# Performance work log

Measured on AMD Instinct MI355X. Metric: run time of the kernel, lower is better.

Reference implementation:

```python
import jax, jax.numpy as jnp
import numpy as np

HIDDEN = 32


def setup_inputs() -> dict:
    key = jax.random.key(0)
    ks = jax.random.split(key, 8)
    B, T, I = 1024, 512, 64
    s_ih = 1.0 / np.sqrt(HIDDEN)
    return {
        "x": jax.random.normal(ks[0], (B, T, I), dtype=jnp.float32),
        "h0": jnp.zeros((1, B, HIDDEN), dtype=jnp.float32),
        "W_ih": jax.random.uniform(ks[1], (HIDDEN, I), jnp.float32, -s_ih, s_ih),
        "b_ih": jax.random.uniform(ks[2], (HIDDEN,), jnp.float32, -s_ih, s_ih),
        "W_hh": jax.random.uniform(ks[3], (HIDDEN, HIDDEN), jnp.float32, -s_ih, s_ih),
        "b_hh": jax.random.uniform(ks[4], (HIDDEN,), jnp.float32, -s_ih, s_ih),
        "W_out": jax.random.uniform(ks[5], (1, HIDDEN), jnp.float32, -s_ih, s_ih),
        "b_out": jax.random.uniform(ks[6], (1,), jnp.float32, -s_ih, s_ih),
    }


def reference(x, h0, W_ih, b_ih, W_hh, b_hh, W_out, b_out):
    # x: [B, T, I]; h0: [1, B, H] (num_layers=1)
    # Precompute input contribution for all timesteps in one GEMM: [B, T, H]
    x_proj = jnp.einsum("bti,hi->bth", x, W_ih) + b_ih

    def step(h, xt):  # h: [B, H], xt: [B, H]
        h_new = jnp.tanh(xt + h @ W_hh.T + b_hh)
        return h_new, h_new

    h_last, r_out_t = jax.lax.scan(step, h0[0], jnp.swapaxes(x_proj, 0, 1))
    r_out = jnp.swapaxes(r_out_t, 0, 1)  # [B, T, H]
    # Per-timestep Linear(32 -> 1), batched as one GEMM: [B, T, 1]
    outs = r_out @ W_out.T + b_out
    return outs, h_last[None]
```

## Files before the change

### kernel.cpp

```cpp
#include <hip/hip_runtime.h>

#define Bc 1024
#define Tc 512
#define Ic 64
#define Hc 32
#define L2E2 2.8853900817779268f

#define XT_ROW 24
#define XT_BUF (Hc * XT_ROW)

typedef __bf16 bf16x8 __attribute__((ext_vector_type(8)));
typedef __bf16 bf16x4 __attribute__((ext_vector_type(4)));
typedef float  f32x4  __attribute__((ext_vector_type(4)));
typedef _Float16 half2v __attribute__((ext_vector_type(2)));
typedef unsigned uint2v __attribute__((ext_vector_type(2)));

__device__ inline bf16x8 to_bf16x8(float4 u0, float4 u1) {
    bf16x8 t;
    t[0] = (__bf16)u0.x; t[1] = (__bf16)u0.y; t[2] = (__bf16)u0.z; t[3] = (__bf16)u0.w;
    t[4] = (__bf16)u1.x; t[5] = (__bf16)u1.y; t[6] = (__bf16)u1.z; t[7] = (__bf16)u1.w;
    return t;
}
__device__ inline bf16x8 to_bf16x8s(float4 u0, float4 u1, float s) {
    bf16x8 t;
    t[0] = (__bf16)(u0.x*s); t[1] = (__bf16)(u0.y*s); t[2] = (__bf16)(u0.z*s); t[3] = (__bf16)(u0.w*s);
    t[4] = (__bf16)(u1.x*s); t[5] = (__bf16)(u1.y*s); t[6] = (__bf16)(u1.z*s); t[7] = (__bf16)(u1.w*s);
    return t;
}


#define RORD(dst, src, N)                                                     \
    dst = (unsigned)__builtin_amdgcn_mov_dpp((int)(src), 0x120 + (N), 0xF, 0xF, false);

#if __has_builtin(__builtin_amdgcn_permlane16_swap)
#define PLSWAP(A, B)                                                          \
    { uint2v _t = __builtin_amdgcn_permlane16_swap((A), (B), false, false);   \
      (A) = _t[0]; (B) = _t[1]; }
#else
#define PLSWAP(A, B)                                                          \
    asm("s_nop 1\n\tv_permlane16_swap_b32 %0, %1" : "+v"(A), "+v"(B));
#endif

#if __has_builtin(__builtin_amdgcn_permlane32_swap)
#define P32SWAP(A, B)                                                         \
    { uint2v _t = __builtin_amdgcn_permlane32_swap((A), (B), false, false);   \
      (A) = _t[0]; (B) = _t[1]; }
#else
#define P32SWAP(A, B)                                                         \
    asm("s_nop 1\n\tv_permlane32_swap_b32 %0, %1" : "+v"(A), "+v"(B));
#endif

#if __has_builtin(__builtin_amdgcn_fdot2)
#define FDOT(g, W, a)                                                         \
    __builtin_amdgcn_fdot2(__builtin_bit_cast(half2v, (unsigned)(g)), (W), (a), false)
#else
__device__ inline float fdot2_emul(unsigned g, half2v w, float a) {
    half2v v = __builtin_bit_cast(half2v, g);
    a = fmaf((float)v[0], (float)w[0], a);
    return fmaf((float)v[1], (float)w[1], a);
}
#define FDOT(g, W, a) fdot2_emul((g), (W), (a))
#endif

#define STEP(xv, uu)                                                          \
    {                                                                         \
        unsigned c8;                                                          \
        RORD(c8, c, 8)                                                        \
        const unsigned bse = rlo ? c : c8;                                    \
        unsigned g1, g2, g3, g4, g5, g6, g7;                                  \
        RORD(g1, bse, 1) RORD(g2, bse, 2) RORD(g3, bse, 3) RORD(g4, bse, 4)   \
        RORD(g5, bse, 5) RORD(g6, bse, 6) RORD(g7, bse, 7)                    \
        float a0 = FDOT(bse, W0, (xv));                                       \
        float a1 = FDOT(g1,  W1, bch);                                        \
        a0 = FDOT(g2, W2, a0);  a1 = FDOT(g3, W3, a1);                        \
        a0 = FDOT(g4, W4, a0);  a1 = FDOT(g5, W5, a1);                        \
        a0 = FDOT(g6, W6, a0);  a1 = FDOT(g7, W7, a1);                        \
        const float Ah = a0 + a1;                                             \
        unsigned sa = __builtin_bit_cast(unsigned, Ah), sb2 = sa;             \
        P32SWAP(sa, sb2)                                                      \
        const float A = __builtin_bit_cast(float, sa) +                       \
                        __builtin_bit_cast(float, sb2);                       \
        const float p_ = __builtin_amdgcn_exp2f(A);                           \
        rr = __builtin_amdgcn_rcpf(p_ + 1.0f);                                \
        pbuf[uu][hh] = fmaf(rr, w2o, wo);                                     \
        unsigned P0 = __builtin_bit_cast(unsigned, rr), P1 = P0;              \
        PLSWAP(P0, P1)                                                        \
        const float rrp = __builtin_bit_cast(float, psel ? P0 : P1);          \
        const float ev = rodd ? rrp : rr;                                     \
        const float od = rodd ? rr : rrp;                                     \
        c = __builtin_bit_cast(unsigned, __builtin_amdgcn_cvt_pkrtz(ev, od)); \
    }

#define CVT8(dlo, dhi, src)                                                   \
    dlo.x = (float)(src)[0]; dlo.y = (float)(src)[1];                         \
    dlo.z = (float)(src)[2]; dlo.w = (float)(src)[3];                         \
    dhi.x = (float)(src)[4]; dhi.y = (float)(src)[5];                         \
    dhi.z = (float)(src)[6]; dhi.w = (float)(src)[7];

#define TILE_LOAD(lt)                                                         \
    do {                                                                      \
        const float* xp_ = x + ((size_t)b * Tc + (lt) * 16 + m2) * Ic + r * 8;\
        Xa0 = ((const float4*)xp_)[0];                                        \
        Xa1 = ((const float4*)xp_)[1];                                        \
        Xa2 = ((const float4*)(xp_ + 32))[0];                                 \
        Xa3 = ((const float4*)(xp_ + 32))[1];                                 \
    } while (0)

#define TILE_MFMA(tp)                                                         \
    do {                                                                      \
        const bf16x8 A0_ = to_bf16x8(Xa0, Xa1);                               \
        const bf16x8 A1_ = to_bf16x8(Xa2, Xa3);                               \
        f32x4 ac0 = {0.f, 0.f, 0.f, 0.f};                                     \
        f32x4 ac1 = {0.f, 0.f, 0.f, 0.f};                                     \
        ac0 = __builtin_amdgcn_mfma_f32_16x16x32_bf16(A0_, Bf[0][0], ac0, 0, 0, 0); \
        ac0 = __builtin_amdgcn_mfma_f32_16x16x32_bf16(A1_, Bf[0][1], ac0, 0, 0, 0); \
        ac1 = __builtin_amdgcn_mfma_f32_16x16x32_bf16(A0_, Bf[1][0], ac1, 0, 0, 0); \
        ac1 = __builtin_amdgcn_mfma_f32_16x16x32_bf16(A1_, Bf[1][1], ac1, 0, 0, 0); \
        bf16x4 p0_, p1_;                                                      \
        p0_[0] = (__bf16)(ac0[0] + bias0); p0_[1] = (__bf16)(ac0[1] + bias0); \
        p0_[2] = (__bf16)(ac0[2] + bias0); p0_[3] = (__bf16)(ac0[3] + bias0); \
        p1_[0] = (__bf16)(ac1[0] + bias1); p1_[1] = (__bf16)(ac1[1] + bias1); \
        p1_[2] = (__bf16)(ac1[2] + bias1); p1_[3] = (__bf16)(ac1[3] + bias1); \
        *(bf16x4*)&(tp)[m2 * XT_ROW + r * 4]        = p0_;                    \
        *(bf16x4*)&(tp)[(m2 + 16) * XT_ROW + r * 4] = p1_;                    \
    } while (0)

__global__ __launch_bounds__(64, 1) void fused_rnn_kernel(
    const float* __restrict__ x, const float* __restrict__ Wih,
    const float* __restrict__ bih, const float* __restrict__ h0,
    const float* __restrict__ Whh, const float* __restrict__ bhh,
    const float* __restrict__ Wout, const float* __restrict__ bout,
    float* __restrict__ out)
{
    __shared__ __bf16 xt[2 * XT_BUF];
    __shared__ float  pbuf[16][36];

    const int lane = threadIdx.x;
    const int m2   = lane & 15;
    const int r    = lane >> 4;
    const bool rlo  = (lane < 32);
    const bool rodd = (r & 1);
    const int  hh   = 2 * m2 + (r & 1);
    const int  b    = blockIdx.x;

    const float shalf = 0.5f * L2E2;
    bf16x8 Bf[2][2];
#pragma unroll
    for (int nh = 0; nh < 2; ++nh)
#pragma unroll
        for (int kh = 0; kh < 2; ++kh) {
            const float* wp = Wih + (m2 + 16 * nh) * Ic + r * 8 + kh * 32;
            Bf[nh][kh] = to_bf16x8s(((const float4*)wp)[0],
                                    ((const float4*)wp)[1], shalf);
        }
    const float bias0 = bih[m2] * shalf;
    const float bias1 = bih[m2 + 16] * shalf;

    bool psel;
    {
        unsigned d0 = (unsigned)lane, d1 = (unsigned)lane;
        PLSWAP(d0, d1)
        psel = (d0 == (unsigned)(lane ^ 16));
    }

    unsigned s0p = (unsigned)(2 * m2) | ((unsigned)(2 * m2 + 1) << 16);
    unsigned s8p;
    RORD(s8p, s0p, 8)
    const unsigned sbp = rlo ? s0p : s8p;
    unsigned sk1, sk2, sk3, sk4, sk5, sk6, sk7;
    RORD(sk1, sbp, 1) RORD(sk2, sbp, 2) RORD(sk3, sbp, 3) RORD(sk4, sbp, 4)
    RORD(sk5, sbp, 5) RORD(sk6, sbp, 6) RORD(sk7, sbp, 7)

    const float cw = -2.0f * L2E2;
    const float* wrh = Whh + hh * Hc;
#define MKW(Wk, sk)                                                           \
    half2v Wk;                                                                \
    {                                                                         \
        const unsigned jl_ = (sk) & 0xFFFFu, jh_ = (sk) >> 16;                \
        Wk[0] = (_Float16)(wrh[jl_] * cw);                                    \
        Wk[1] = (_Float16)(wrh[jh_] * cw);                                    \
    }
    MKW(W0, sbp) MKW(W1, sk1) MKW(W2, sk2) MKW(W3, sk3)
    MKW(W4, sk4) MKW(W5, sk5) MKW(W6, sk6) MKW(W7, sk7)
#undef MKW

    float rs = 0.f;
#pragma unroll
    for (int j = 0; j < Hc; ++j) rs += wrh[j];
    const float bch = (bhh[hh] + rs) * shalf;
    const float wo  = Wout[hh];
    const float w2o = -2.0f * wo;
    const float bo  = bout[0];

    const float h0e = h0[(size_t)b * Hc + 2 * m2];
    const float h0o = h0[(size_t)b * Hc + 2 * m2 + 1];
    const float re0 = fmaf(-0.5f, h0e, 0.5f);
    const float ro0 = fmaf(-0.5f, h0o, 0.5f);
    unsigned c = __builtin_bit_cast(unsigned, __builtin_amdgcn_cvt_pkrtz(re0, ro0));
    float rr = rodd ? ro0 : re0;
    float* orow = out + (size_t)b * Tc;

    float4 Xa0, Xa1, Xa2, Xa3;
    TILE_LOAD(0);
    TILE_MFMA(xt);
    TILE_LOAD(1);
    TILE_MFMA(xt + XT_BUF);
    TILE_LOAD(2);
    __syncthreads();

    const __bf16* xrbase = xt + hh * XT_ROW;

    bf16x8 na0 = *(const bf16x8*)(xrbase), na1 = *(const bf16x8*)(xrbase + 8);
    float4 qa0, qa1, qa2, qa3;
    CVT8(qa0, qa1, na0) CVT8(qa2, qa3, na1)

#pragma unroll 1
    for (int tb = 0; tb < Tc / 16; ++tb) {
        const int tbn = (tb + 1 < Tc / 16) ? tb + 1 : tb;
        const __bf16* xr = xrbase + (tbn & 1) * XT_BUF;
        na0 = *(const bf16x8*)(xr); na1 = *(const bf16x8*)(xr + 8);

        if (tb + 2 < Tc / 16) { TILE_MFMA(xt + (tb & 1) * XT_BUF); }
        if (tb + 3 < Tc / 16) { TILE_LOAD(tb + 3); }

        STEP(qa0.x, 0)  STEP(qa0.y, 1)  STEP(qa0.z, 2)  STEP(qa0.w, 3)
        STEP(qa1.x, 4)  STEP(qa1.y, 5)  STEP(qa1.z, 6)  STEP(qa1.w, 7)
        STEP(qa2.x, 8)  STEP(qa2.y, 9)  STEP(qa2.z, 10) STEP(qa2.w, 11)
        STEP(qa3.x, 12) STEP(qa3.y, 13) STEP(qa3.z, 14) STEP(qa3.w, 15)

        __builtin_amdgcn_wave_barrier();

        if (lane < 16) {
            const float4* pr = (const float4*)&pbuf[lane][0];
            const float4 s0_ = pr[0], s1_ = pr[1], s2_ = pr[2], s3_ = pr[3];
            const float4 s4_ = pr[4], s5_ = pr[5], s6_ = pr[6], s7_ = pr[7];
            const float s =
                ((((s0_.x + s0_.y) + (s0_.z + s0_.w)) +
                  ((s1_.x + s1_.y) + (s1_.z + s1_.w))) +
                 (((s2_.x + s2_.y) + (s2_.z + s2_.w)) +
                  ((s3_.x + s3_.y) + (s3_.z + s3_.w)))) +
                ((((s4_.x + s4_.y) + (s4_.z + s4_.w)) +
                  ((s5_.x + s5_.y) + (s5_.z + s5_.w))) +
                 (((s6_.x + s6_.y) + (s6_.z + s6_.w)) +
                  ((s7_.x + s7_.y) + (s7_.z + s7_.w))));
            orow[tb * 16 + lane] = s + bo;
        }
        __builtin_amdgcn_wave_barrier();

        CVT8(qa0, qa1, na0) CVT8(qa2, qa3, na1)
    }

    out[(size_t)Bc * Tc + (size_t)b * Hc + hh] = fmaf(-2.0f, rr, 1.0f);
}

extern "C" void kernel_launch(void* const* d_in, const int* in_sizes, int n_in,
                              void* d_out, int out_size, void* d_ws, size_t ws_size,
                              hipStream_t stream) {
    const float* x    = (const float*)d_in[0];
    const float* h0   = (const float*)d_in[1];
    const float* Wih  = (const float*)d_in[2];
    const float* bih  = (const float*)d_in[3];
    const float* Whh  = (const float*)d_in[4];
    const float* bhh  = (const float*)d_in[5];
    const float* Wout = (const float*)d_in[6];
    const float* bout = (const float*)d_in[7];
    float* out = (float*)d_out;

    fused_rnn_kernel<<<Bc, 64, 0, stream>>>(x, Wih, bih, h0, Whh, bhh,
                                            Wout, bout, out);
}
```

Measured before the change: 225.2 us.

## Split recurrence and projection into producer/consumer waves with fp32 DPP dot

Launches two waves per block. Wave 1 produces the bf16 MFMA input projection and reduces the output linear for the previous tile, while wave 0 runs only the serial recurrence. The recurrence now uses full-fp32 FMAs on 32 lanes with DPP rotations and a permlane16 swap, in place of packed fp16 dot products followed by a cross-half permlane32 reduction. This takes the projection and output work off the serial critical path and removes the half-precision packing. In exchange it adds a block-wide __syncthreads every 16 timesteps and more DPP moves per step.

```diff
diff --git a/kernel.cpp b/kernel.cpp
--- a/kernel.cpp
+++ b/kernel.cpp
@@ -12,7 +12,6 @@
 typedef __bf16 bf16x8 __attribute__((ext_vector_type(8)));
 typedef __bf16 bf16x4 __attribute__((ext_vector_type(4)));
 typedef float  f32x4  __attribute__((ext_vector_type(4)));
-typedef _Float16 half2v __attribute__((ext_vector_type(2)));
 typedef unsigned uint2v __attribute__((ext_vector_type(2)));
 
 __device__ inline bf16x8 to_bf16x8(float4 u0, float4 u1) {
@@ -41,54 +40,60 @@
     asm("s_nop 1\n\tv_permlane16_swap_b32 %0, %1" : "+v"(A), "+v"(B));
 #endif
 
-#if __has_builtin(__builtin_amdgcn_permlane32_swap)
-#define P32SWAP(A, B)                                                         \
-    { uint2v _t = __builtin_amdgcn_permlane32_swap((A), (B), false, false);   \
-      (A) = _t[0]; (B) = _t[1]; }
-#else
-#define P32SWAP(A, B)                                                         \
-    asm("s_nop 1\n\tv_permlane32_swap_b32 %0, %1" : "+v"(A), "+v"(B));
-#endif
-
-#if __has_builtin(__builtin_amdgcn_fdot2)
-#define FDOT(g, W, a)                                                         \
-    __builtin_amdgcn_fdot2(__builtin_bit_cast(half2v, (unsigned)(g)), (W), (a), false)
-#else
-__device__ inline float fdot2_emul(unsigned g, half2v w, float a) {
-    half2v v = __builtin_bit_cast(half2v, g);
-    a = fmaf((float)v[0], (float)w[0], a);
-    return fmaf((float)v[1], (float)w[1], a);
-}
-#define FDOT(g, W, a) fdot2_emul((g), (W), (a))
-#endif
+#define F32(u) __builtin_bit_cast(float, (u))
 
 #define STEP(xv, uu)                                                          \
     {                                                                         \
-        unsigned c8;                                                          \
-        RORD(c8, c, 8)                                                        \
-        const unsigned bse = rlo ? c : c8;                                    \
-        unsigned g1, g2, g3, g4, g5, g6, g7;                                  \
-        RORD(g1, bse, 1) RORD(g2, bse, 2) RORD(g3, bse, 3) RORD(g4, bse, 4)   \
-        RORD(g5, bse, 5) RORD(g6, bse, 6) RORD(g7, bse, 7)                    \
-        float a0 = FDOT(bse, W0, (xv));                                       \
-        float a1 = FDOT(g1,  W1, bch);                                        \
-        a0 = FDOT(g2, W2, a0);  a1 = FDOT(g3, W3, a1);                        \
-        a0 = FDOT(g4, W4, a0);  a1 = FDOT(g5, W5, a1);                        \
-        a0 = FDOT(g6, W6, a0);  a1 = FDOT(g7, W7, a1);                        \
-        const float Ah = a0 + a1;                                             \
-        unsigned sa = __builtin_bit_cast(unsigned, Ah), sb2 = sa;             \
-        P32SWAP(sa, sb2)                                                      \
-        const float A = __builtin_bit_cast(float, sa) +                       \
-                        __builtin_bit_cast(float, sb2);                       \
-        const float p_ = __builtin_amdgcn_exp2f(A);                           \
-        rr = __builtin_amdgcn_rcpf(p_ + 1.0f);                                \
-        pbuf[uu][hh] = fmaf(rr, w2o, wo);                                     \
-        unsigned P0 = __builtin_bit_cast(unsigned, rr), P1 = P0;              \
-        PLSWAP(P0, P1)                                                        \
-        const float rrp = __builtin_bit_cast(float, psel ? P0 : P1);          \
-        const float ev = rodd ? rrp : rr;                                     \
-        const float od = rodd ? rr : rrp;                                     \
-        c = __builtin_bit_cast(unsigned, __builtin_amdgcn_cvt_pkrtz(ev, od)); \
+        unsigned P0_ = c, P1_ = c;                                            \
+        PLSWAP(P0_, P1_)                                                      \
+        const unsigned cp = psel ? P0_ : P1_;                                 \
+        unsigned o1,o2,o3,o4,o5,o6,o7,o8,o9,o10,o11,o12,o13,o14,o15;          \
+        unsigned p1,p2,p3,p4,p5,p6,p7,p8,p9,p10,p11,p12,p13,p14,p15;          \
+        RORD(o1,c,1)  RORD(o2,c,2)   RORD(o3,c,3)   RORD(o4,c,4)              \
+        RORD(o5,c,5)  RORD(o6,c,6)   RORD(o7,c,7)   RORD(o8,c,8)              \
+        RORD(o9,c,9)  RORD(o10,c,10) RORD(o11,c,11) RORD(o12,c,12)            \
+        RORD(o13,c,13) RORD(o14,c,14) RORD(o15,c,15)                          \
+        RORD(p1,cp,1)  RORD(p2,cp,2)   RORD(p3,cp,3)   RORD(p4,cp,4)          \
+        RORD(p5,cp,5)  RORD(p6,cp,6)   RORD(p7,cp,7)   RORD(p8,cp,8)          \
+        RORD(p9,cp,9)  RORD(p10,cp,10) RORD(p11,cp,11) RORD(p12,cp,12)        \
+        RORD(p13,cp,13) RORD(p14,cp,14) RORD(p15,cp,15)                       \
+        float a0 = fmaf(F32(c), Wo0, (xv));                                   \
+        a0 = fmaf(F32(o1), Wo1, a0);                                          \
+        a0 = fmaf(F32(o2), Wo2, a0);                                          \
+        a0 = fmaf(F32(o3), Wo3, a0);                                          \
+        float a1 = F32(o4) * Wo4;                                             \
+        a1 = fmaf(F32(o5), Wo5, a1);                                          \
+        a1 = fmaf(F32(o6), Wo6, a1);                                          \
+        a1 = fmaf(F32(o7), Wo7, a1);                                          \
+        float a2 = F32(o8) * Wo8;                                             \
+        a2 = fmaf(F32(o9),  Wo9,  a2);                                        \
+        a2 = fmaf(F32(o10), Wo10, a2);                                        \
+        a2 = fmaf(F32(o11), Wo11, a2);                                        \
+        float a3 = F32(o12) * Wo12;                                           \
+        a3 = fmaf(F32(o13), Wo13, a3);                                        \
+        a3 = fmaf(F32(o14), Wo14, a3);                                        \
+        a3 = fmaf(F32(o15), Wo15, a3);                                        \
+        float a4 = fmaf(F32(cp), Wp0, bch);                                   \
+        a4 = fmaf(F32(p1), Wp1, a4);                                          \
+        a4 = fmaf(F32(p2), Wp2, a4);                                          \
+        a4 = fmaf(F32(p3), Wp3, a4);                                          \
+        float a5 = F32(p4) * Wp4;                                             \
+        a5 = fmaf(F32(p5), Wp5, a5);                                          \
+        a5 = fmaf(F32(p6), Wp6, a5);                                          \
+        a5 = fmaf(F32(p7), Wp7, a5);                                          \
+        float a6 = F32(p8) * Wp8;                                             \
+        a6 = fmaf(F32(p9),  Wp9,  a6);                                        \
+        a6 = fmaf(F32(p10), Wp10, a6);                                        \
+        a6 = fmaf(F32(p11), Wp11, a6);                                        \
+        float a7 = F32(p12) * Wp12;                                           \
+        a7 = fmaf(F32(p13), Wp13, a7);                                        \
+        a7 = fmaf(F32(p14), Wp14, a7);                                        \
+        a7 = fmaf(F32(p15), Wp15, a7);                                        \
+        const float A_ = ((a0 + a1) + (a2 + a3)) + ((a4 + a5) + (a6 + a7));   \
+        const float e_ = __builtin_amdgcn_exp2f(A_);                          \
+        rr = __builtin_amdgcn_rcpf(e_ + 1.0f);                                \
+        pb[(uu) * 36] = fmaf(rr, w2o, wo);                                    \
+        c = __builtin_bit_cast(unsigned, rr);                                 \
     }
 
 #define CVT8(dlo, dhi, src)                                                   \
@@ -125,7 +130,7 @@
         *(bf16x4*)&(tp)[(m2 + 16) * XT_ROW + r * 4] = p1_;                    \
     } while (0)
 
-__global__ __launch_bounds__(64, 1) void fused_rnn_kernel(
+__global__ __launch_bounds__(128, 1) void fused_rnn_kernel(
     const float* __restrict__ x, const float* __restrict__ Wih,
     const float* __restrict__ bih, const float* __restrict__ h0,
     const float* __restrict__ Whh, const float* __restrict__ bhh,
@@ -133,124 +138,158 @@
     float* __restrict__ out)
 {
     __shared__ __bf16 xt[2 * XT_BUF];
-    __shared__ float  pbuf[16][36];
-
-    const int lane = threadIdx.x;
+    __shared__ float  pbuf[2][16][36];
+
+    const int tid  = threadIdx.x;
+    const int wid  = tid >> 6;
+    const int lane = tid & 63;
     const int m2   = lane & 15;
     const int r    = lane >> 4;
-    const bool rlo  = (lane < 32);
-    const bool rodd = (r & 1);
-    const int  hh   = 2 * m2 + (r & 1);
-    const int  b    = blockIdx.x;
-
-    const float shalf = 0.5f * L2E2;
+    const int h31  = lane & 31;
+    const int b    = blockIdx.x;
+
     bf16x8 Bf[2][2];
+    float  bias0 = 0.f, bias1 = 0.f;
+    float4 Xa0, Xa1, Xa2, Xa3;
+    bool  psel = false;
+    float Wo0=0,Wo1=0,Wo2=0,Wo3=0,Wo4=0,Wo5=0,Wo6=0,Wo7=0,
+          Wo8=0,Wo9=0,Wo10=0,Wo11=0,Wo12=0,Wo13=0,Wo14=0,Wo15=0,
+          Wp0=0,Wp1=0,Wp2=0,Wp3=0,Wp4=0,Wp5=0,Wp6=0,Wp7=0,
+          Wp8=0,Wp9=0,Wp10=0,Wp11=0,Wp12=0,Wp13=0,Wp14=0,Wp15=0;
+    float bch = 0.f, wo = 0.f, w2o = 0.f, rr = 0.f;
+    unsigned c = 0;
+    bf16x8 na0, na1;
+    float4 qa0, qa1, qa2, qa3;
+    const float bo = bout[0];
+    float* orow = out + (size_t)b * Tc;
+    const __bf16* xrbase = xt + h31 * XT_ROW;
+
+    if (wid == 1) {
 #pragma unroll
-    for (int nh = 0; nh < 2; ++nh)
+        for (int nh = 0; nh < 2; ++nh)
 #pragma unroll
-        for (int kh = 0; kh < 2; ++kh) {
-            const float* wp = Wih + (m2 + 16 * nh) * Ic + r * 8 + kh * 32;
-            Bf[nh][kh] = to_bf16x8s(((const float4*)wp)[0],
-                                    ((const float4*)wp)[1], shalf);
+            for (int kh = 0; kh < 2; ++kh) {
+                const float* wp = Wih + (m2 + 16 * nh) * Ic + r * 8 + kh * 32;
+                Bf[nh][kh] = to_bf16x8s(((const float4*)wp)[0],
+                                        ((const float4*)wp)[1], L2E2);
+            }
+        bias0 = bih[m2] * L2E2;
+        bias1 = bih[m2 + 16] * L2E2;
+        TILE_LOAD(0); TILE_MFMA(xt);
+        TILE_LOAD(1); TILE_MFMA(xt + XT_BUF);
+        TILE_LOAD(2);
+    } else {
+        {
+            unsigned d0 = (unsigned)lane, d1 = (unsigned)lane;
+            PLSWAP(d0, d1)
+            psel = (d0 == (unsigned)(lane ^ 16));
         }
-    const float bias0 = bih[m2] * shalf;
-    const float bias1 = bih[m2 + 16] * shalf;
-
-    bool psel;
-    {
-        unsigned d0 = (unsigned)lane, d1 = (unsigned)lane;
-        PLSWAP(d0, d1)
-        psel = (d0 == (unsigned)(lane ^ 16));
-    }
-
-    unsigned s0p = (unsigned)(2 * m2) | ((unsigned)(2 * m2 + 1) << 16);
-    unsigned s8p;
-    RORD(s8p, s0p, 8)
-    const unsigned sbp = rlo ? s0p : s8p;
-    unsigned sk1, sk2, sk3, sk4, sk5, sk6, sk7;
-    RORD(sk1, sbp, 1) RORD(sk2, sbp, 2) RORD(sk3, sbp, 3) RORD(sk4, sbp, 4)
-    RORD(sk5, sbp, 5) RORD(sk6, sbp, 6) RORD(sk7, sbp, 7)
-
-    const float cw = -2.0f * L2E2;
-    const float* wrh = Whh + hh * Hc;
-#define MKW(Wk, sk)                                                           \
-    half2v Wk;                                                                \
-    {                                                                         \
-        const unsigned jl_ = (sk) & 0xFFFFu, jh_ = (sk) >> 16;                \
-        Wk[0] = (_Float16)(wrh[jl_] * cw);                                    \
-        Wk[1] = (_Float16)(wrh[jh_] * cw);                                    \
-    }
-    MKW(W0, sbp) MKW(W1, sk1) MKW(W2, sk2) MKW(W3, sk3)
-    MKW(W4, sk4) MKW(W5, sk5) MKW(W6, sk6) MKW(W7, sk7)
-#undef MKW
-
-    float rs = 0.f;
+        const unsigned u = (unsigned)h31;
+        unsigned up;
+        { unsigned U0 = u, U1 = u; PLSWAP(U0, U1) up = psel ? U0 : U1; }
+        unsigned so1,so2,so3,so4,so5,so6,so7,so8,so9,so10,so11,so12,so13,so14,so15;
+        unsigned sp1,sp2,sp3,sp4,sp5,sp6,sp7,sp8,sp9,sp10,sp11,sp12,sp13,sp14,sp15;
+        RORD(so1,u,1)  RORD(so2,u,2)   RORD(so3,u,3)   RORD(so4,u,4)
+        RORD(so5,u,5)  RORD(so6,u,6)   RORD(so7,u,7)   RORD(so8,u,8)
+        RORD(so9,u,9)  RORD(so10,u,10) RORD(so11,u,11) RORD(so12,u,12)
+        RORD(so13,u,13) RORD(so14,u,14) RORD(so15,u,15)
+        RORD(sp1,up,1)  RORD(sp2,up,2)   RORD(sp3,up,3)   RORD(sp4,up,4)
+        RORD(sp5,up,5)  RORD(sp6,up,6)   RORD(sp7,up,7)   RORD(sp8,up,8)
+        RORD(sp9,up,9)  RORD(sp10,up,10) RORD(sp11,up,11) RORD(sp12,up,12)
+        RORD(sp13,up,13) RORD(sp14,up,14) RORD(sp15,up,15)
+        const float cw = -2.0f * L2E2;
+        const float* wrh = Whh + h31 * Hc;
+        Wo0  = wrh[u]    * cw;
+        Wo1  = wrh[so1]  * cw;  Wo2  = wrh[so2]  * cw;
+        Wo3  = wrh[so3]  * cw;  Wo4  = wrh[so4]  * cw;
+        Wo5  = wrh[so5]  * cw;  Wo6  = wrh[so6]  * cw;
+        Wo7  = wrh[so7]  * cw;  Wo8  = wrh[so8]  * cw;
+        Wo9  = wrh[so9]  * cw;  Wo10 = wrh[so10] * cw;
+        Wo11 = wrh[so11] * cw;  Wo12 = wrh[so12] * cw;
+        Wo13 = wrh[so13] * cw;  Wo14 = wrh[so14] * cw;
+        Wo15 = wrh[so15] * cw;
+        Wp0  = wrh[up]   * cw;
+        Wp1  = wrh[sp1]  * cw;  Wp2  = wrh[sp2]  * cw;
+        Wp3  = wrh[sp3]  * cw;  Wp4  = wrh[sp4]  * cw;
+        Wp5  = wrh[sp5]  * cw;  Wp6  = wrh[sp6]  * cw;
+        Wp7  = wrh[sp7]  * cw;  Wp8  = wrh[sp8]  * cw;
+        Wp9  = wrh[sp9]  * cw;  Wp10 = wrh[sp10] * cw;
+        Wp11 = wrh[sp11] * cw;  Wp12 = wrh[sp12] * cw;
+        Wp13 = wrh[sp13] * cw;  Wp14 = wrh[sp14] * cw;
+        Wp15 = wrh[sp15] * cw;
+        float rs = 0.f;
 #pragma unroll
-    for (int j = 0; j < Hc; ++j) rs += wrh[j];
-    const float bch = (bhh[hh] + rs) * shalf;
-    const float wo  = Wout[hh];
-    const float w2o = -2.0f * wo;
-    const float bo  = bout[0];
-
-    const float h0e = h0[(size_t)b * Hc + 2 * m2];
-    const float h0o = h0[(size_t)b * Hc + 2 * m2 + 1];
-    const float re0 = fmaf(-0.5f, h0e, 0.5f);
-    const float ro0 = fmaf(-0.5f, h0o, 0.5f);
-    unsigned c = __builtin_bit_cast(unsigned, __builtin_amdgcn_cvt_pkrtz(re0, ro0));
-    float rr = rodd ? ro0 : re0;
-    float* orow = out + (size_t)b * Tc;
-
-    float4 Xa0, Xa1, Xa2, Xa3;
-    TILE_LOAD(0);
-    TILE_MFMA(xt);
-    TILE_LOAD(1);
-    TILE_MFMA(xt + XT_BUF);
-    TILE_LOAD(2);
+        for (int j = 0; j < Hc; ++j) rs += wrh[j];
+        bch = (bhh[h31] + rs) * L2E2;
+        wo  = Wout[h31];
+        w2o = -2.0f * wo;
+        rr = fmaf(-0.5f, h0[(size_t)b * Hc + h31], 0.5f);
+        c  = __builtin_bit_cast(unsigned, rr);
+    }
     __syncthreads();
 
-    const __bf16* xrbase = xt + hh * XT_ROW;
-
-    bf16x8 na0 = *(const bf16x8*)(xrbase), na1 = *(const bf16x8*)(xrbase + 8);
-    float4 qa0, qa1, qa2, qa3;
-    CVT8(qa0, qa1, na0) CVT8(qa2, qa3, na1)
+    if (wid == 0) {
+        na0 = *(const bf16x8*)(xrbase);
+        na1 = *(const bf16x8*)(xrbase + 8);
+        CVT8(qa0, qa1, na0) CVT8(qa2, qa3, na1)
+    }
+    __syncthreads();
 
 #pragma unroll 1
     for (int tb = 0; tb < Tc / 16; ++tb) {
-        const int tbn = (tb + 1 < Tc / 16) ? tb + 1 : tb;
-        const __bf16* xr = xrbase + (tbn & 1) * XT_BUF;
-        na0 = *(const bf16x8*)(xr); na1 = *(const bf16x8*)(xr + 8);
-
-        if (tb + 2 < Tc / 16) { TILE_MFMA(xt + (tb & 1) * XT_BUF); }
-        if (tb + 3 < Tc / 16) { TILE_LOAD(tb + 3); }
-
-        STEP(qa0.x, 0)  STEP(qa0.y, 1)  STEP(qa0.z, 2)  STEP(qa0.w, 3)
-        STEP(qa1.x, 4)  STEP(qa1.y, 5)  STEP(qa1.z, 6)  STEP(qa1.w, 7)
-        STEP(qa2.x, 8)  STEP(qa2.y, 9)  STEP(qa2.z, 10) STEP(qa2.w, 11)
-        STEP(qa3.x, 12) STEP(qa3.y, 13) STEP(qa3.z, 14) STEP(qa3.w, 15)
-
-        __builtin_amdgcn_wave_barrier();
-
-        if (lane < 16) {
-            const float4* pr = (const float4*)&pbuf[lane][0];
-            const float4 s0_ = pr[0], s1_ = pr[1], s2_ = pr[2], s3_ = pr[3];
-            const float4 s4_ = pr[4], s5_ = pr[5], s6_ = pr[6], s7_ = pr[7];
-            const float s =
-                ((((s0_.x + s0_.y) + (s0_.z + s0_.w)) +
-                  ((s1_.x + s1_.y) + (s1_.z + s1_.w))) +
-                 (((s2_.x + s2_.y) + (s2_.z + s2_.w)) +
-                  ((s3_.x + s3_.y) + (s3_.z + s3_.w)))) +
-                ((((s4_.x + s4_.y) + (s4_.z + s4_.w)) +
-                  ((s5_.x + s5_.y) + (s5_.z + s5_.w))) +
-                 (((s6_.x + s6_.y) + (s6_.z + s6_.w)) +
-                  ((s7_.x + s7_.y) + (s7_.z + s7_.w))));
-            orow[tb * 16 + lane] = s + bo;
+        if (wid == 0) {
+            const int tbn = (tb + 1 < Tc / 16) ? tb + 1 : tb;
+            const __bf16* xr = xrbase + (tbn & 1) * XT_BUF;
+            na0 = *(const bf16x8*)(xr);
+            na1 = *(const bf16x8*)(xr + 8);
+
+            float* pb = &pbuf[tb & 1][0][h31];
+            STEP(qa0.x, 0)  STEP(qa0.y, 1)  STEP(qa0.z, 2)  STEP(qa0.w, 3)
+            STEP(qa1.x, 4)  STEP(qa1.y, 5)  STEP(qa1.z, 6)  STEP(qa1.w, 7)
+            STEP(qa2.x, 8)  STEP(qa2.y, 9)  STEP(qa2.z, 10) STEP(qa2.w, 11)
+            STEP(qa3.x, 12) STEP(qa3.y, 13) STEP(qa3.z, 14) STEP(qa3.w, 15)
+
+            CVT8(qa0, qa1, na0) CVT8(qa2, qa3, na1)
+        } else {
+            if (tb + 2 < Tc / 16) { TILE_MFMA(xt + (tb & 1) * XT_BUF); }
+            if (tb + 3 < Tc / 16) { TILE_LOAD(tb + 3); }
+            if (tb >= 1 && lane < 16) {
+                const float4* pr = (const float4*)&pbuf[(tb - 1) & 1][lane][0];
+                const float4 s0_ = pr[0], s1_ = pr[1], s2_ = pr[2], s3_ = pr[3];
+                const float4 s4_ = pr[4], s5_ = pr[5], s6_ = pr[6], s7_ = pr[7];
+                const float s =
+                    ((((s0_.x + s0_.y) + (s0_.z + s0_.w)) +
+                      ((s1_.x + s1_.y) + (s1_.z + s1_.w))) +
+                     (((s2_.x + s2_.y) + (s2_.z + s2_.w)) +
+                      ((s3_.x + s3_.y) + (s3_.z + s3_.w)))) +
+                    ((((s4_.x + s4_.y) + (s4_.z + s4_.w)) +
+                      ((s5_.x + s5_.y) + (s5_.z + s5_.w))) +
+                     (((s6_.x + s6_.y) + (s6_.z + s6_.w)) +
+                      ((s7_.x + s7_.y) + (s7_.z + s7_.w))));
+                orow[(tb - 1) * 16 + lane] = s + bo;
+            }
         }
-        __builtin_amdgcn_wave_barrier();
-
-        CVT8(qa0, qa1, na0) CVT8(qa2, qa3, na1)
-    }
-
-    out[(size_t)Bc * Tc + (size_t)b * Hc + hh] = fmaf(-2.0f, rr, 1.0f);
+        __syncthreads();
+    }
+
+    if (wid == 1 && lane < 16) {
+        const float4* pr = (const float4*)&pbuf[(Tc / 16 - 1) & 1][lane][0];
+        const float4 s0_ = pr[0], s1_ = pr[1], s2_ = pr[2], s3_ = pr[3];
+        const float4 s4_ = pr[4], s5_ = pr[5], s6_ = pr[6], s7_ = pr[7];
+        const float s =
+            ((((s0_.x + s0_.y) + (s0_.z + s0_.w)) +
+              ((s1_.x + s1_.y) + (s1_.z + s1_.w))) +
+             (((s2_.x + s2_.y) + (s2_.z + s2_.w)) +
+              ((s3_.x + s3_.y) + (s3_.z + s3_.w)))) +
+            ((((s4_.x + s4_.y) + (s4_.z + s4_.w)) +
+              ((s5_.x + s5_.y) + (s5_.z + s5_.w))) +
+             (((s6_.x + s6_.y) + (s6_.z + s6_.w)) +
+              ((s7_.x + s7_.y) + (s7_.z + s7_.w))));
+        orow[(Tc / 16 - 1) * 16 + lane] = s + bo;
+    }
+    if (wid == 0 && lane < 32) {
+        out[(size_t)Bc * Tc + (size_t)b * Hc + lane] = fmaf(-2.0f, rr, 1.0f);
+    }
 }
 
 extern "C" void kernel_launch(void* const* d_in, const int* in_sizes, int n_in,
@@ -266,6 +305,6 @@
     const float* bout = (const float*)d_in[7];
     float* out = (float*)d_out;
 
-    fused_rnn_kernel<<<Bc, 64, 0, stream>>>(x, Wih, bih, h0, Whh, bhh,
-                                            Wout, bout, out);
+    fused_rnn_kernel<<<Bc, 128, 0, stream>>>(x, Wih, bih, h0, Whh, bhh,
+                                             Wout, bout, out);
 }
```

Result: slower. 236.0 us (+4.8%).

## Compute full recurrent dot per lane with 16 DPP rotations, drop cross-half swap

Applied to the files above, without the earlier changes.

Each lane now computes the whole 32-element recurrent dot product itself, using 15 row-rotate DPP moves and 16 fdot2 ops across four accumulator chains. Previously the two wave halves each computed half the sum and combined them with a permlane32 swap. This removes the cross-half exchange and add from the serial per-timestep critical path, and the 0.5 scale factors are folded into L2E2. The cost is more DPP and fdot2 work per step, plus redundant computation across the two halves, so only lanes below 32 write the final hidden state.

```diff
diff --git a/kernel.cpp b/kernel.cpp
--- a/kernel.cpp
+++ b/kernel.cpp
@@ -41,15 +41,6 @@
     asm("s_nop 1\n\tv_permlane16_swap_b32 %0, %1" : "+v"(A), "+v"(B));
 #endif
 
-#if __has_builtin(__builtin_amdgcn_permlane32_swap)
-#define P32SWAP(A, B)                                                         \
-    { uint2v _t = __builtin_amdgcn_permlane32_swap((A), (B), false, false);   \
-      (A) = _t[0]; (B) = _t[1]; }
-#else
-#define P32SWAP(A, B)                                                         \
-    asm("s_nop 1\n\tv_permlane32_swap_b32 %0, %1" : "+v"(A), "+v"(B));
-#endif
-
 #if __has_builtin(__builtin_amdgcn_fdot2)
 #define FDOT(g, W, a)                                                         \
     __builtin_amdgcn_fdot2(__builtin_bit_cast(half2v, (unsigned)(g)), (W), (a), false)
@@ -64,23 +55,23 @@
 
 #define STEP(xv, uu)                                                          \
     {                                                                         \
-        unsigned c8;                                                          \
-        RORD(c8, c, 8)                                                        \
-        const unsigned bse = rlo ? c : c8;                                    \
-        unsigned g1, g2, g3, g4, g5, g6, g7;                                  \
-        RORD(g1, bse, 1) RORD(g2, bse, 2) RORD(g3, bse, 3) RORD(g4, bse, 4)   \
-        RORD(g5, bse, 5) RORD(g6, bse, 6) RORD(g7, bse, 7)                    \
-        float a0 = FDOT(bse, W0, (xv));                                       \
-        float a1 = FDOT(g1,  W1, bch);                                        \
-        a0 = FDOT(g2, W2, a0);  a1 = FDOT(g3, W3, a1);                        \
-        a0 = FDOT(g4, W4, a0);  a1 = FDOT(g5, W5, a1);                        \
-        a0 = FDOT(g6, W6, a0);  a1 = FDOT(g7, W7, a1);                        \
-        const float Ah = a0 + a1;                                             \
-        unsigned sa = __builtin_bit_cast(unsigned, Ah), sb2 = sa;             \
-        P32SWAP(sa, sb2)                                                      \
-        const float A = __builtin_bit_cast(float, sa) +                       \
-                        __builtin_bit_cast(float, sb2);                       \
-        const float p_ = __builtin_amdgcn_exp2f(A);                           \
+        unsigned g1,g2,g3,g4,g5,g6,g7,g8,g9,g10,g11,g12,g13,g14,g15;          \
+        RORD(g1,c,1)   RORD(g2,c,2)   RORD(g3,c,3)   RORD(g4,c,4)             \
+        RORD(g5,c,5)   RORD(g6,c,6)   RORD(g7,c,7)   RORD(g8,c,8)             \
+        RORD(g9,c,9)   RORD(g10,c,10) RORD(g11,c,11) RORD(g12,c,12)           \
+        RORD(g13,c,13) RORD(g14,c,14) RORD(g15,c,15)                          \
+        float a0 = FDOT(c,  W0, (xv));                                        \
+        float a1 = FDOT(g1, W1, bch);                                         \
+        float a2 = FDOT(g2, W2, 0.0f);                                        \
+        float a3 = FDOT(g3, W3, 0.0f);                                        \
+        a0 = FDOT(g4,  W4,  a0);  a1 = FDOT(g5,  W5,  a1);                    \
+        a2 = FDOT(g6,  W6,  a2);  a3 = FDOT(g7,  W7,  a3);                    \
+        a0 = FDOT(g8,  W8,  a0);  a1 = FDOT(g9,  W9,  a1);                    \
+        a2 = FDOT(g10, W10, a2);  a3 = FDOT(g11, W11, a3);                    \
+        a0 = FDOT(g12, W12, a0);  a1 = FDOT(g13, W13, a1);                    \
+        a2 = FDOT(g14, W14, a2);  a3 = FDOT(g15, W15, a3);                    \
+        const float A_ = (a0 + a1) + (a2 + a3);                               \
+        const float p_ = __builtin_amdgcn_exp2f(A_);                          \
         rr = __builtin_amdgcn_rcpf(p_ + 1.0f);                                \
         pbuf[uu][hh] = fmaf(rr, w2o, wo);                                     \
         unsigned P0 = __builtin_bit_cast(unsigned, rr), P1 = P0;              \
@@ -138,12 +129,10 @@
     const int lane = threadIdx.x;
     const int m2   = lane & 15;
     const int r    = lane >> 4;
-    const bool rlo  = (lane < 32);
     const bool rodd = (r & 1);
     const int  hh   = 2 * m2 + (r & 1);
     const int  b    = blockIdx.x;
 
-    const float shalf = 0.5f * L2E2;
     bf16x8 Bf[2][2];
 #pragma unroll
     for (int nh = 0; nh < 2; ++nh)
@@ -151,10 +140,10 @@
         for (int kh = 0; kh < 2; ++kh) {
             const float* wp = Wih + (m2 + 16 * nh) * Ic + r * 8 + kh * 32;
             Bf[nh][kh] = to_bf16x8s(((const float4*)wp)[0],
-                                    ((const float4*)wp)[1], shalf);
+                                    ((const float4*)wp)[1], L2E2);
         }
-    const float bias0 = bih[m2] * shalf;
-    const float bias1 = bih[m2 + 16] * shalf;
+    const float bias0 = bih[m2] * L2E2;
+    const float bias1 = bih[m2 + 16] * L2E2;
 
     bool psel;
     {
@@ -164,12 +153,13 @@
     }
 
     unsigned s0p = (unsigned)(2 * m2) | ((unsigned)(2 * m2 + 1) << 16);
-    unsigned s8p;
-    RORD(s8p, s0p, 8)
-    const unsigned sbp = rlo ? s0p : s8p;
-    unsigned sk1, sk2, sk3, sk4, sk5, sk6, sk7;
-    RORD(sk1, sbp, 1) RORD(sk2, sbp, 2) RORD(sk3, sbp, 3) RORD(sk4, sbp, 4)
-    RORD(sk5, sbp, 5) RORD(sk6, sbp, 6) RORD(sk7, sbp, 7)
+    unsigned sk1, sk2, sk3, sk4, sk5, sk6, sk7, sk8, sk9, sk10, sk11, sk12,
+             sk13, sk14, sk15;
+    RORD(sk1, s0p, 1)   RORD(sk2, s0p, 2)   RORD(sk3, s0p, 3)
+    RORD(sk4, s0p, 4)   RORD(sk5, s0p, 5)   RORD(sk6, s0p, 6)
+    RORD(sk7, s0p, 7)   RORD(sk8, s0p, 8)   RORD(sk9, s0p, 9)
+    RORD(sk10, s0p, 10) RORD(sk11, s0p, 11) RORD(sk12, s0p, 12)
+    RORD(sk13, s0p, 13) RORD(sk14, s0p, 14) RORD(sk15, s0p, 15)
 
     const float cw = -2.0f * L2E2;
     const float* wrh = Whh + hh * Hc;
@@ -180,14 +170,16 @@
         Wk[0] = (_Float16)(wrh[jl_] * cw);                                    \
         Wk[1] = (_Float16)(wrh[jh_] * cw);                                    \
     }
-    MKW(W0, sbp) MKW(W1, sk1) MKW(W2, sk2) MKW(W3, sk3)
-    MKW(W4, sk4) MKW(W5, sk5) MKW(W6, sk6) MKW(W7, sk7)
+    MKW(W0, s0p)  MKW(W1, sk1)  MKW(W2, sk2)   MKW(W3, sk3)
+    MKW(W4, sk4)  MKW(W5, sk5)  MKW(W6, sk6)   MKW(W7, sk7)
+    MKW(W8, sk8)  MKW(W9, sk9)  MKW(W10, sk10) MKW(W11, sk11)
+    MKW(W12, sk12) MKW(W13, sk13) MKW(W14, sk14) MKW(W15, sk15)
 #undef MKW
 
     float rs = 0.f;
 #pragma unroll
     for (int j = 0; j < Hc; ++j) rs += wrh[j];
-    const float bch = (bhh[hh] + rs) * shalf;
+    const float bch = (bhh[hh] + rs) * L2E2;
     const float wo  = Wout[hh];
     const float w2o = -2.0f * wo;
     const float bo  = bout[0];
@@ -250,7 +242,9 @@
         CVT8(qa0, qa1, na0) CVT8(qa2, qa3, na1)
     }
 
-    out[(size_t)Bc * Tc + (size_t)b * Hc + hh] = fmaf(-2.0f, rr, 1.0f);
+    if (lane < 32) {
+        out[(size_t)Bc * Tc + (size_t)b * Hc + hh] = fmaf(-2.0f, rr, 1.0f);
+    }
 }
 
 extern "C" void kernel_launch(void* const* d_in, const int* in_sizes, int n_in,
```

New measurement: 229.4 us. No clear change (+1.8%).
